# Kernel optimization log

Hardware: AMD Instinct MI355X
Metric: run time of the kernel (lower is better)

Reference implementation:

```python
import jax, jax.numpy as jnp
import numpy as np

TIME_STEP = 32
BATCH = 1048576


def setup_inputs() -> dict:
    key = jax.random.key(0)
    k_x, k_w, k_b = jax.random.split(key, 3)
    inputs = jax.random.normal(k_x, (BATCH, TIME_STEP), dtype=jnp.float32)
    # Row t of W holds the weights of nn.Linear(t+1, 1); entries j>t are unused (masked).
    # Match torch Linear init scale: U(-1/sqrt(fan_in), 1/sqrt(fan_in)) per row, roughly -> just use small uniform.
    W = jax.random.uniform(k_w, (TIME_STEP, TIME_STEP), dtype=jnp.float32, minval=-0.5, maxval=0.5)
    b = jax.random.uniform(k_b, (TIME_STEP,), dtype=jnp.float32, minval=-0.5, maxval=0.5)
    return {"inputs": inputs, "W": W, "b": b}


def reference(inputs, W, b):
    # out[n, t] = sum_{j <= t} W[t, j] * inputs[n, j] + b[t]
    # Fuse the T tiny linears into one triangular-masked matmul.
    Wtri = jnp.tril(W)                       # [T, T] lower triangular
    return jnp.einsum("nj,tj->nt", inputs, Wtri) + b  # [B, T]
```

## Files before the change

### kernel.cpp

```cpp
#include <hip/hip_runtime.h>


constexpr int T    = 32;
constexpr int ROWS = 256;
constexpr int RSTR = T + 1;

__global__ __launch_bounds__(256) void triu_kernel(
    const float* __restrict__ x, const float* __restrict__ W,
    const float* __restrict__ b, float* __restrict__ out)
{
    __shared__ float sW[T * T];
    __shared__ float sb[T];
    __shared__ float sX[ROWS * RSTR];

    const int tid = threadIdx.x;

    #pragma unroll
    for (int i = tid; i < T * T; i += 256) sW[i] = W[i];
    if (tid < T) sb[tid] = b[tid];

    const long long base = (long long)blockIdx.x * (ROWS * T);

    const float4* __restrict__ x4 = reinterpret_cast<const float4*>(x + base);
    #pragma unroll
    for (int it = 0; it < (ROWS * T) / (256 * 4); ++it) {
        const int idx = it * 256 + tid;
        const float4 v = x4[idx];
        const int row = idx >> 3;
        const int col = (idx & 7) << 2;
        const int p = row * RSTR + col;
        sX[p + 0] = v.x; sX[p + 1] = v.y; sX[p + 2] = v.z; sX[p + 3] = v.w;
    }
    __syncthreads();

    float acc[T];
    #pragma unroll
    for (int t = 0; t < T; ++t) acc[t] = sb[t];

    float* myrow = &sX[tid * RSTR];
    #pragma unroll
    for (int j = 0; j < T; ++j) {
        const float xj = myrow[j];
        #pragma unroll
        for (int t = j; t < T; ++t)
            acc[t] = fmaf(sW[t * T + j], xj, acc[t]);
    }

    #pragma unroll
    for (int t = 0; t < T; ++t) myrow[t] = acc[t];
    __syncthreads();

    float4* __restrict__ o4 = reinterpret_cast<float4*>(out + base);
    #pragma unroll
    for (int it = 0; it < 8; ++it) {
        const int idx = it * 256 + tid;
        const int row = idx >> 3;
        const int col = (idx & 7) << 2;
        const int p = row * RSTR + col;
        o4[idx] = make_float4(sX[p + 0], sX[p + 1], sX[p + 2], sX[p + 3]);
    }
}

extern "C" void kernel_launch(void* const* d_in, const int* in_sizes, int n_in,
                              void* d_out, int out_size, void* d_ws, size_t ws_size,
                              hipStream_t stream) {
    const float* x  = (const float*)d_in[0];
    const float* W  = (const float*)d_in[1];
    const float* b  = (const float*)d_in[2];
    float* out      = (float*)d_out;

    const int batch = in_sizes[0] / T;
    const int grid  = batch / ROWS;
    triu_kernel<<<grid, 256, 0, stream>>>(x, W, b, out);
}
```

Before: 238.6 us.

## Process two rows per thread and load triangular weights as float4 from LDS

Doubles the rows per block to 512 so each thread computes two output rows. The triangular weights are read from shared memory as float4 in 4-column chunks and reused across both rows, which cuts LDS weight traffic per FMA. It also adds a min-blocks hint to launch_bounds. In exchange, LDS use per block roughly doubles (about 68KB) and register pressure rises from 64 accumulators, which can lower occupancy for what is a memory-bound kernel.

```diff
diff --git a/kernel.cpp b/kernel.cpp
--- a/kernel.cpp
+++ b/kernel.cpp
@@ -1,11 +1,11 @@
 #include <hip/hip_runtime.h>
 
 
-constexpr int T    = 32;
-constexpr int ROWS = 256;
-constexpr int RSTR = T + 1;
+constexpr int T     = 32;
+constexpr int ROWS  = 512;
+constexpr int RSTR  = T + 1;
 
-__global__ __launch_bounds__(256) void triu_kernel(
+__global__ __launch_bounds__(256, 2) void triu_kernel(
     const float* __restrict__ x, const float* __restrict__ W,
     const float* __restrict__ b, float* __restrict__ out)
 {
@@ -15,49 +15,75 @@
 
     const int tid = threadIdx.x;
 
-    #pragma unroll
     for (int i = tid; i < T * T; i += 256) sW[i] = W[i];
     if (tid < T) sb[tid] = b[tid];
 
     const long long base = (long long)blockIdx.x * (ROWS * T);
+    const float4* __restrict__ x4 = reinterpret_cast<const float4*>(x + base);
 
-    const float4* __restrict__ x4 = reinterpret_cast<const float4*>(x + base);
     #pragma unroll
     for (int it = 0; it < (ROWS * T) / (256 * 4); ++it) {
         const int idx = it * 256 + tid;
         const float4 v = x4[idx];
-        const int row = idx >> 3;
-        const int col = (idx & 7) << 2;
-        const int p = row * RSTR + col;
-        sX[p + 0] = v.x; sX[p + 1] = v.y; sX[p + 2] = v.z; sX[p + 3] = v.w;
+        const int r = idx >> 3;
+        const int c = (idx & 7) << 2;
+        float* p = &sX[r * RSTR + c];
+        p[0] = v.x; p[1] = v.y; p[2] = v.z; p[3] = v.w;
     }
     __syncthreads();
 
-    float acc[T];
+    float acc0[T], acc1[T];
     #pragma unroll
-    for (int t = 0; t < T; ++t) acc[t] = sb[t];
+    for (int t = 0; t < T; ++t) { const float bt = sb[t]; acc0[t] = bt; acc1[t] = bt; }
 
-    float* myrow = &sX[tid * RSTR];
+    const float* __restrict__ r0 = &sX[tid * RSTR];
+    const float* __restrict__ r1 = &sX[(tid + 256) * RSTR];
+
     #pragma unroll
-    for (int j = 0; j < T; ++j) {
-        const float xj = myrow[j];
+    for (int jc = 0; jc < 8; ++jc) {
+        float a0[4], a1[4];
         #pragma unroll
-        for (int t = j; t < T; ++t)
-            acc[t] = fmaf(sW[t * T + j], xj, acc[t]);
+        for (int k = 0; k < 4; ++k) { a0[k] = r0[4 * jc + k]; a1[k] = r1[4 * jc + k]; }
+
+        #pragma unroll
+        for (int k = 0; k < 4; ++k) {
+            const int t = 4 * jc + k;
+            const float4 w4 = *reinterpret_cast<const float4*>(&sW[t * T + 4 * jc]);
+            const float wv[4] = {w4.x, w4.y, w4.z, w4.w};
+            #pragma unroll
+            for (int j = 0; j <= k; ++j) {
+                acc0[t] = fmaf(wv[j], a0[j], acc0[t]);
+                acc1[t] = fmaf(wv[j], a1[j], acc1[t]);
+            }
+        }
+        #pragma unroll
+        for (int t = 4 * jc + 4; t < T; ++t) {
+            const float4 w4 = *reinterpret_cast<const float4*>(&sW[t * T + 4 * jc]);
+            acc0[t] = fmaf(w4.x, a0[0], acc0[t]);
+            acc0[t] = fmaf(w4.y, a0[1], acc0[t]);
+            acc0[t] = fmaf(w4.z, a0[2], acc0[t]);
+            acc0[t] = fmaf(w4.w, a0[3], acc0[t]);
+            acc1[t] = fmaf(w4.x, a1[0], acc1[t]);
+            acc1[t] = fmaf(w4.y, a1[1], acc1[t]);
+            acc1[t] = fmaf(w4.z, a1[2], acc1[t]);
+            acc1[t] = fmaf(w4.w, a1[3], acc1[t]);
+        }
     }
 
+    float* w0 = &sX[tid * RSTR];
+    float* w1 = &sX[(tid + 256) * RSTR];
     #pragma unroll
-    for (int t = 0; t < T; ++t) myrow[t] = acc[t];
+    for (int t = 0; t < T; ++t) { w0[t] = acc0[t]; w1[t] = acc1[t]; }
     __syncthreads();
 
     float4* __restrict__ o4 = reinterpret_cast<float4*>(out + base);
     #pragma unroll
-    for (int it = 0; it < 8; ++it) {
+    for (int it = 0; it < (ROWS * T) / (256 * 4); ++it) {
         const int idx = it * 256 + tid;
-        const int row = idx >> 3;
-        const int col = (idx & 7) << 2;
-        const int p = row * RSTR + col;
-        o4[idx] = make_float4(sX[p + 0], sX[p + 1], sX[p + 2], sX[p + 3]);
+        const int r = idx >> 3;
+        const int c = (idx & 7) << 2;
+        const float* p = &sX[r * RSTR + c];
+        o4[idx] = make_float4(p[0], p[1], p[2], p[3]);
     }
 }
 
```

Result: slower. 250.2 us (+4.8%).
